# Kernel tuning notes

Measured on AMD Instinct MI355X. Metric: run time of the kernel, lower is better.

Reference implementation:

```python
import jax, jax.numpy as jnp
import numpy as np

EPS = 1e-6


def setup_inputs() -> dict:
    key = jax.random.key(0)
    k1, k2, k3 = jax.random.split(key, 3)
    B, L, H, D = 4, 4096, 16, 64
    return {
        "queries": jax.random.normal(k1, (B, L, H, D), dtype=jnp.float32),
        "keys": jax.random.normal(k2, (B, L, H, D), dtype=jnp.float32),
        "values": jax.random.normal(k3, (B, L, H, D), dtype=jnp.float32),
        "attn_mask": jnp.zeros((1,), dtype=bool),  # unused, matches torch signature
    }


def reference(queries, keys, values, attn_mask):
    # [B, L, H, D] -> [B, H, L, D]
    q = jax.nn.sigmoid(jnp.transpose(queries, (0, 2, 1, 3)))
    k = jax.nn.sigmoid(jnp.transpose(keys, (0, 2, 1, 3)))
    v = jnp.transpose(values, (0, 2, 1, 3))
    L = q.shape[2]
    S = k.shape[2]

    # flow normalizers (incoming / outgoing)
    normalizer_row = 1.0 / jnp.einsum('nhld,nhd->nhl', q + EPS, k.sum(axis=2) + EPS)
    normalizer_col = 1.0 / jnp.einsum('nhsd,nhd->nhs', k + EPS, q.sum(axis=2) + EPS)

    # competitive refinement
    row_refine = jnp.einsum(
        'nhld,nhd->nhl', q + EPS, (k * normalizer_col[..., None]).sum(axis=2) + EPS)
    col_refine = jnp.einsum(
        'nhsd,nhd->nhs', k + EPS, (q * normalizer_row[..., None]).sum(axis=2) + EPS)
    row_refine = jax.nn.sigmoid(row_refine * (float(L) / float(S)))
    col_refine = jax.nn.softmax(col_refine, axis=-1) * S

    # kv: [B, H, D, D]
    kv = jnp.einsum('nhsd,nhse->nhde', k, v * col_refine[..., None])
    x = jnp.einsum('nhld,nhde->nhle', q, kv)
    x = x * normalizer_row[..., None] * row_refine[..., None]
    # back to [B, L, H, D]
    return jnp.transpose(x, (0, 2, 1, 3))
```

## Files before the change

kernel.cpp:

```cpp
#include <hip/hip_runtime.h>
#include <math.h>
#include <stdint.h>

#define B_ 4
#define L_ 4096
#define H_ 16
#define EPSF 1e-6f
#define STR 66
#define STRO 68

typedef short bf16x8 __attribute__((ext_vector_type(8)));
typedef float f32x4 __attribute__((ext_vector_type(4)));
union FragU { uint32_t u[4]; bf16x8 v; };

__device__ __forceinline__ float sigf(float x) { return 1.0f / (1.0f + __expf(-x)); }

__device__ __forceinline__ uint32_t packhl(float x) {
    uint32_t xb = __float_as_uint(x);
    uint32_t hb = xb & 0xFFFF0000u;
    float lo = x - __uint_as_float(hb);
    return (hb >> 16) | (__float_as_uint(lo) & 0xFFFF0000u);
}

__device__ __forceinline__ void buildfrag(const uint32_t w[8], bf16x8& hi, bf16x8& lo) {
    FragU H, L;
#pragma unroll
    for (int t = 0; t < 4; ++t) {
        H.u[t] = __builtin_amdgcn_perm(w[2 * t + 1], w[2 * t], 0x05040100u);
        L.u[t] = __builtin_amdgcn_perm(w[2 * t + 1], w[2 * t], 0x07060302u);
    }
    hi = H.v; lo = L.v;
}

#define MFMA3(acc, ahi, alo, bhi, blo)                                        \
    acc = __builtin_amdgcn_mfma_f32_16x16x32_bf16(ahi, bhi, acc, 0, 0, 0);    \
    acc = __builtin_amdgcn_mfma_f32_16x16x32_bf16(ahi, blo, acc, 0, 0, 0);    \
    acc = __builtin_amdgcn_mfma_f32_16x16x32_bf16(alo, bhi, acc, 0, 0, 0);

__global__ __launch_bounds__(256) void k_ksum(const float* __restrict__ K,
                                              float* __restrict__ ksum) {
    int bh = blockIdx.x, b = bh >> 4, h = bh & 15;
    int t = threadIdx.x, lane = t & 63, w = t >> 6;
    int q4 = lane >> 4, i16 = lane & 15;
    int r0 = blockIdx.y * 256 + w * 64;
    float a0 = 0.f, a1 = 0.f, a2 = 0.f, a3 = 0.f;
    for (int it = 0; it < 16; ++it) {
        int r = r0 + it * 4 + q4;
        float4 x = *(const float4*)(K + (((size_t)b * L_ + r) * H_ + h) * 64 + 4 * i16);
        a0 += sigf(x.x); a1 += sigf(x.y); a2 += sigf(x.z); a3 += sigf(x.w);
    }
#pragma unroll
    for (int m = 16; m < 64; m <<= 1) {
        a0 += __shfl_xor(a0, m, 64); a1 += __shfl_xor(a1, m, 64);
        a2 += __shfl_xor(a2, m, 64); a3 += __shfl_xor(a3, m, 64);
    }
    if (q4 == 0) {
        atomicAdd(&ksum[bh * 64 + 4 * i16 + 0], a0);
        atomicAdd(&ksum[bh * 64 + 4 * i16 + 1], a1);
        atomicAdd(&ksum[bh * 64 + 4 * i16 + 2], a2);
        atomicAdd(&ksum[bh * 64 + 4 * i16 + 3], a3);
    }
}

__global__ __launch_bounds__(256) void k_qpass(const float* __restrict__ Q,
                                               const float* __restrict__ ksum,
                                               float* __restrict__ qsum,
                                               float* __restrict__ qn) {
    int bh = blockIdx.x, b = bh >> 4, h = bh & 15;
    int t = threadIdx.x, lane = t & 63, w = t >> 6;
    int q4 = lane >> 4, i16 = lane & 15;
    int r0 = blockIdx.y * 256 + w * 64;
    float4 ks4 = *(const float4*)(ksum + bh * 64 + 4 * i16);
    ks4.x += EPSF; ks4.y += EPSF; ks4.z += EPSF; ks4.w += EPSF;
    float qs0 = 0.f, qs1 = 0.f, qs2 = 0.f, qs3 = 0.f;
    float qa0 = 0.f, qa1 = 0.f, qa2 = 0.f, qa3 = 0.f;
    for (int it = 0; it < 16; ++it) {
        int r = r0 + it * 4 + q4;
        float4 x = *(const float4*)(Q + (((size_t)b * L_ + r) * H_ + h) * 64 + 4 * i16);
        float s0 = sigf(x.x), s1 = sigf(x.y), s2 = sigf(x.z), s3 = sigf(x.w);
        float pa = (s0 + EPSF) * ks4.x + (s1 + EPSF) * ks4.y +
                   (s2 + EPSF) * ks4.z + (s3 + EPSF) * ks4.w;
#pragma unroll
        for (int m = 1; m < 16; m <<= 1) pa += __shfl_xor(pa, m, 64);
        float nr = __builtin_amdgcn_rcpf(pa);
        qs0 += s0; qs1 += s1; qs2 += s2; qs3 += s3;
        qa0 += s0 * nr; qa1 += s1 * nr; qa2 += s2 * nr; qa3 += s3 * nr;
    }
#pragma unroll
    for (int m = 16; m < 64; m <<= 1) {
        qs0 += __shfl_xor(qs0, m, 64); qs1 += __shfl_xor(qs1, m, 64);
        qs2 += __shfl_xor(qs2, m, 64); qs3 += __shfl_xor(qs3, m, 64);
        qa0 += __shfl_xor(qa0, m, 64); qa1 += __shfl_xor(qa1, m, 64);
        qa2 += __shfl_xor(qa2, m, 64); qa3 += __shfl_xor(qa3, m, 64);
    }
    if (q4 == 0) {
        atomicAdd(&qsum[bh * 64 + 4 * i16 + 0], qs0);
        atomicAdd(&qsum[bh * 64 + 4 * i16 + 1], qs1);
        atomicAdd(&qsum[bh * 64 + 4 * i16 + 2], qs2);
        atomicAdd(&qsum[bh * 64 + 4 * i16 + 3], qs3);
        atomicAdd(&qn[bh * 64 + 4 * i16 + 0], qa0);
        atomicAdd(&qn[bh * 64 + 4 * i16 + 1], qa1);
        atomicAdd(&qn[bh * 64 + 4 * i16 + 2], qa2);
        atomicAdd(&qn[bh * 64 + 4 * i16 + 3], qa3);
    }
}

__global__ __launch_bounds__(256) void k_kv(const float* __restrict__ K,
                                            const float* __restrict__ V,
                                            const float* __restrict__ qsum,
                                            const float* __restrict__ qn,
                                            float* __restrict__ kn,
                                            float* __restrict__ den,
                                            float* __restrict__ KVg) {
    int bh = blockIdx.x, b = bh >> 4, h = bh & 15;
    int t = threadIdx.x, lane = t & 63, w = t >> 6;
    int q4 = lane >> 4, i16 = lane & 15;
    __shared__ uint32_t skp[64 * STR];
    __shared__ uint32_t vwp[64 * STR];
    float4 qsE = *(const float4*)(qsum + bh * 64 + 4 * i16);
    float4 qnE = *(const float4*)(qn + bh * 64 + 4 * i16);
    qsE.x += EPSF; qsE.y += EPSF; qsE.z += EPSF; qsE.w += EPSF;
    qnE.x += EPSF; qnE.y += EPSF; qnE.z += EPSF; qnE.w += EPSF;
    f32x4 acc[4];
#pragma unroll
    for (int tm = 0; tm < 4; ++tm) acc[tm] = (f32x4){0.f, 0.f, 0.f, 0.f};
    float kn0 = 0.f, kn1 = 0.f, kn2 = 0.f, kn3 = 0.f, dacc = 0.f;
    int rowbase = blockIdx.y * 256;
    for (int tile = 0; tile < 4; ++tile) {
#pragma unroll
        for (int j = 0; j < 4; ++j) {
            int lr = w * 16 + j * 4 + q4;
            int r = rowbase + tile * 64 + lr;
            size_t off = (((size_t)b * L_ + r) * H_ + h) * 64 + 4 * i16;
            float4 kx = *(const float4*)(K + off);
            float s0 = sigf(kx.x), s1 = sigf(kx.y), s2 = sigf(kx.z), s3 = sigf(kx.w);
            float pa = (s0 + EPSF) * qsE.x + (s1 + EPSF) * qsE.y +
                       (s2 + EPSF) * qsE.z + (s3 + EPSF) * qsE.w;
            float pc = (s0 + EPSF) * qnE.x + (s1 + EPSF) * qnE.y +
                       (s2 + EPSF) * qnE.z + (s3 + EPSF) * qnE.w;
#pragma unroll
            for (int m = 1; m < 16; m <<= 1) {
                pa += __shfl_xor(pa, m, 64);
                pc += __shfl_xor(pc, m, 64);
            }
            float ncol = __builtin_amdgcn_rcpf(pa);
            float es = __expf(pc);
            kn0 += s0 * ncol; kn1 += s1 * ncol; kn2 += s2 * ncol; kn3 += s3 * ncol;
            if (i16 == 0) dacc += es;
            uint32_t* sp = &skp[lr * STR + 4 * i16];
            *(uint2*)sp = make_uint2(packhl(s0), packhl(s1));
            *(uint2*)(sp + 2) = make_uint2(packhl(s2), packhl(s3));
            float4 vx = *(const float4*)(V + off);
            uint32_t* vp = &vwp[lr * STR + 4 * i16];
            *(uint2*)vp = make_uint2(packhl(vx.x * es), packhl(vx.y * es));
            *(uint2*)(vp + 2) = make_uint2(packhl(vx.z * es), packhl(vx.w * es));
        }
        __syncthreads();
#pragma unroll
        for (int ks = 0; ks < 2; ++ks) {
            uint32_t bw[8];
#pragma unroll
            for (int j = 0; j < 8; ++j)
                bw[j] = vwp[(32 * ks + 8 * q4 + j) * STR + 16 * w + i16];
            bf16x8 bhi, blo; buildfrag(bw, bhi, blo);
#pragma unroll
            for (int tm = 0; tm < 4; ++tm) {
                uint32_t aw[8];
#pragma unroll
                for (int j = 0; j < 8; ++j)
                    aw[j] = skp[(32 * ks + 8 * q4 + j) * STR + 16 * tm + i16];
                bf16x8 ahi, alo; buildfrag(aw, ahi, alo);
                MFMA3(acc[tm], ahi, alo, bhi, blo);
            }
        }
        __syncthreads();
    }
#pragma unroll
    for (int tm = 0; tm < 4; ++tm)
#pragma unroll
        for (int r = 0; r < 4; ++r)
            atomicAdd(&KVg[(size_t)bh * 4096 + (16 * tm + 4 * q4 + r) * 64 + 16 * w + i16],
                      acc[tm][r]);
#pragma unroll
    for (int m = 16; m < 64; m <<= 1) {
        kn0 += __shfl_xor(kn0, m, 64); kn1 += __shfl_xor(kn1, m, 64);
        kn2 += __shfl_xor(kn2, m, 64); kn3 += __shfl_xor(kn3, m, 64);
    }
    if (q4 == 0) {
        atomicAdd(&kn[bh * 64 + 4 * i16 + 0], kn0);
        atomicAdd(&kn[bh * 64 + 4 * i16 + 1], kn1);
        atomicAdd(&kn[bh * 64 + 4 * i16 + 2], kn2);
        atomicAdd(&kn[bh * 64 + 4 * i16 + 3], kn3);
    }
#pragma unroll
    for (int m = 1; m < 64; m <<= 1) dacc += __shfl_xor(dacc, m, 64);
    if (lane == 0) atomicAdd(&den[bh], dacc);
}

__global__ __launch_bounds__(256) void k_out(const float* __restrict__ Q,
                                             const float* __restrict__ ksum,
                                             const float* __restrict__ kn,
                                             const float* __restrict__ den,
                                             const float* __restrict__ KVg,
                                             float* __restrict__ out) {
    int bh = blockIdx.x, b = bh >> 4, h = bh & 15;
    int t = threadIdx.x, lane = t & 63, w = t >> 6;
    int q4 = lane >> 4, i16 = lane & 15;
    __shared__ uint32_t kvt[64 * STRO];
    __shared__ uint32_t sqp[4][16 * STRO];
    __shared__ float scale_s[4][16];
    float4 ksE = *(const float4*)(ksum + bh * 64 + 4 * i16);
    float4 knE = *(const float4*)(kn + bh * 64 + 4 * i16);
    ksE.x += EPSF; ksE.y += EPSF; ksE.z += EPSF; ksE.w += EPSF;
    knE.x += EPSF; knE.y += EPSF; knE.z += EPSF; knE.w += EPSF;
    float sden = 4096.0f * __builtin_amdgcn_rcpf(den[bh]);
    for (int idx = t; idx < 4096; idx += 256) {
        float x = KVg[(size_t)bh * 4096 + idx];
        kvt[(idx & 63) * STRO + (idx >> 6)] = packhl(x);
    }
    __syncthreads();
    int rowbase = blockIdx.y * 256;
    for (int g = 0; g < 4; ++g) {
        int r0 = rowbase + w * 64 + g * 16;
#pragma unroll
        for (int j = 0; j < 4; ++j) {
            int lr = j * 4 + q4;
            int r = r0 + lr;
            float4 qx = *(const float4*)(Q + (((size_t)b * L_ + r) * H_ + h) * 64 + 4 * i16);
            float s0 = sigf(qx.x), s1 = sigf(qx.y), s2 = sigf(qx.z), s3 = sigf(qx.w);
            float pa = (s0 + EPSF) * ksE.x + (s1 + EPSF) * ksE.y +
                       (s2 + EPSF) * ksE.z + (s3 + EPSF) * ksE.w;
            float pb = (s0 + EPSF) * knE.x + (s1 + EPSF) * knE.y +
                       (s2 + EPSF) * knE.z + (s3 + EPSF) * knE.w;
#pragma unroll
            for (int m = 1; m < 16; m <<= 1) {
                pa += __shfl_xor(pa, m, 64);
                pb += __shfl_xor(pb, m, 64);
            }
            float sc = __builtin_amdgcn_rcpf(pa) * sigf(pb) * sden;
            if (i16 == 0) scale_s[w][lr] = sc;
            uint32_t* sp = &sqp[w][lr * STRO + 4 * i16];
            *(uint4*)sp = make_uint4(packhl(s0), packhl(s1), packhl(s2), packhl(s3));
        }
        f32x4 acc[4];
#pragma unroll
        for (int tn = 0; tn < 4; ++tn) acc[tn] = (f32x4){0.f, 0.f, 0.f, 0.f};
#pragma unroll
        for (int ks = 0; ks < 2; ++ks) {
            const uint32_t* ap = &sqp[w][i16 * STRO + 32 * ks + 8 * q4];
            uint4 a0 = *(const uint4*)ap, a1 = *(const uint4*)(ap + 4);
            uint32_t aw[8] = {a0.x, a0.y, a0.z, a0.w, a1.x, a1.y, a1.z, a1.w};
            bf16x8 ahi, alo; buildfrag(aw, ahi, alo);
#pragma unroll
            for (int tn = 0; tn < 4; ++tn) {
                const uint32_t* bp = &kvt[(16 * tn + i16) * STRO + 32 * ks + 8 * q4];
                uint4 b0 = *(const uint4*)bp, b1 = *(const uint4*)(bp + 4);
                uint32_t bw[8] = {b0.x, b0.y, b0.z, b0.w, b1.x, b1.y, b1.z, b1.w};
                bf16x8 bhi, blo; buildfrag(bw, bhi, blo);
                MFMA3(acc[tn], ahi, alo, bhi, blo);
            }
        }
#pragma unroll
        for (int tn = 0; tn < 4; ++tn)
#pragma unroll
            for (int r = 0; r < 4; ++r) {
                int rl = 4 * q4 + r;
                float sc = scale_s[w][rl];
                out[(((size_t)b * L_ + (r0 + rl)) * H_ + h) * 64 + 16 * tn + i16] =
                    acc[tn][r] * sc;
            }
    }
}

extern "C" void kernel_launch(void* const* d_in, const int* in_sizes, int n_in,
                              void* d_out, int out_size, void* d_ws, size_t ws_size,
                              hipStream_t stream) {
    const float* Q = (const float*)d_in[0];
    const float* K = (const float*)d_in[1];
    const float* V = (const float*)d_in[2];
    float* out = (float*)d_out;
    float* ws = (float*)d_ws;
    float* ksum = ws;
    float* qsum = ws + 4096;
    float* qn   = ws + 8192;
    float* kn   = ws + 12288;
    float* den  = ws + 16384;
    float* KVg  = ws + 16448;

    hipMemsetAsync(d_ws, 0, (16448ull + 262144ull) * 4ull, stream);
    k_ksum<<<dim3(64, 16), 256, 0, stream>>>(K, ksum);
    k_qpass<<<dim3(64, 16), 256, 0, stream>>>(Q, ksum, qsum, qn);
    k_kv<<<dim3(64, 16), 256, 0, stream>>>(K, V, qsum, qn, kn, den, KVg);
    k_out<<<dim3(64, 16), 256, 0, stream>>>(Q, ksum, kn, den, KVg, out);
}
```

Baseline: 309.5 us.

## Prefetch tiles in registers, replace KV atomics with partial-sum reduce, double grid

Doubles the grid for the ksum/qpass kernels with batched float4 loads to raise memory-level parallelism. k_kv and k_out now prefetch the next tile's K/V or Q into registers while the current tile computes. The KV atomicAdd accumulation is replaced by per-block partial slices plus a separate reduce kernel, which also shrinks the memset. Adds launch-bounds occupancy hints, an extra kernel launch, 4 MB more workspace traffic, and more register pressure.

```diff
diff --git a/kernel.cpp b/kernel.cpp
--- a/kernel.cpp
+++ b/kernel.cpp
@@ -37,17 +37,26 @@
     acc = __builtin_amdgcn_mfma_f32_16x16x32_bf16(ahi, blo, acc, 0, 0, 0);    \
     acc = __builtin_amdgcn_mfma_f32_16x16x32_bf16(alo, bhi, acc, 0, 0, 0);
 
-__global__ __launch_bounds__(256) void k_ksum(const float* __restrict__ K,
-                                              float* __restrict__ ksum) {
+__global__ __launch_bounds__(256, 8) void k_ksum(const float* __restrict__ K,
+                                                 float* __restrict__ ksum) {
     int bh = blockIdx.x, b = bh >> 4, h = bh & 15;
     int t = threadIdx.x, lane = t & 63, w = t >> 6;
     int q4 = lane >> 4, i16 = lane & 15;
-    int r0 = blockIdx.y * 256 + w * 64;
+    int r0 = blockIdx.y * 128 + w * 32;
     float a0 = 0.f, a1 = 0.f, a2 = 0.f, a3 = 0.f;
-    for (int it = 0; it < 16; ++it) {
-        int r = r0 + it * 4 + q4;
-        float4 x = *(const float4*)(K + (((size_t)b * L_ + r) * H_ + h) * 64 + 4 * i16);
-        a0 += sigf(x.x); a1 += sigf(x.y); a2 += sigf(x.z); a3 += sigf(x.w);
+#pragma unroll
+    for (int ib = 0; ib < 2; ++ib) {
+        float4 x[4];
+#pragma unroll
+        for (int j = 0; j < 4; ++j) {
+            int r = r0 + (ib * 4 + j) * 4 + q4;
+            x[j] = *(const float4*)(K + (((size_t)b * L_ + r) * H_ + h) * 64 + 4 * i16);
+        }
+#pragma unroll
+        for (int j = 0; j < 4; ++j) {
+            a0 += sigf(x[j].x); a1 += sigf(x[j].y);
+            a2 += sigf(x[j].z); a3 += sigf(x[j].w);
+        }
     }
 #pragma unroll
     for (int m = 16; m < 64; m <<= 1) {
@@ -62,29 +71,37 @@
     }
 }
 
-__global__ __launch_bounds__(256) void k_qpass(const float* __restrict__ Q,
-                                               const float* __restrict__ ksum,
-                                               float* __restrict__ qsum,
-                                               float* __restrict__ qn) {
+__global__ __launch_bounds__(256, 6) void k_qpass(const float* __restrict__ Q,
+                                                  const float* __restrict__ ksum,
+                                                  float* __restrict__ qsum,
+                                                  float* __restrict__ qn) {
     int bh = blockIdx.x, b = bh >> 4, h = bh & 15;
     int t = threadIdx.x, lane = t & 63, w = t >> 6;
     int q4 = lane >> 4, i16 = lane & 15;
-    int r0 = blockIdx.y * 256 + w * 64;
+    int r0 = blockIdx.y * 128 + w * 32;
     float4 ks4 = *(const float4*)(ksum + bh * 64 + 4 * i16);
     ks4.x += EPSF; ks4.y += EPSF; ks4.z += EPSF; ks4.w += EPSF;
     float qs0 = 0.f, qs1 = 0.f, qs2 = 0.f, qs3 = 0.f;
     float qa0 = 0.f, qa1 = 0.f, qa2 = 0.f, qa3 = 0.f;
-    for (int it = 0; it < 16; ++it) {
-        int r = r0 + it * 4 + q4;
-        float4 x = *(const float4*)(Q + (((size_t)b * L_ + r) * H_ + h) * 64 + 4 * i16);
-        float s0 = sigf(x.x), s1 = sigf(x.y), s2 = sigf(x.z), s3 = sigf(x.w);
-        float pa = (s0 + EPSF) * ks4.x + (s1 + EPSF) * ks4.y +
-                   (s2 + EPSF) * ks4.z + (s3 + EPSF) * ks4.w;
-#pragma unroll
-        for (int m = 1; m < 16; m <<= 1) pa += __shfl_xor(pa, m, 64);
-        float nr = __builtin_amdgcn_rcpf(pa);
-        qs0 += s0; qs1 += s1; qs2 += s2; qs3 += s3;
-        qa0 += s0 * nr; qa1 += s1 * nr; qa2 += s2 * nr; qa3 += s3 * nr;
+#pragma unroll
+    for (int ib = 0; ib < 2; ++ib) {
+        float4 x[4];
+#pragma unroll
+        for (int j = 0; j < 4; ++j) {
+            int r = r0 + (ib * 4 + j) * 4 + q4;
+            x[j] = *(const float4*)(Q + (((size_t)b * L_ + r) * H_ + h) * 64 + 4 * i16);
+        }
+#pragma unroll
+        for (int j = 0; j < 4; ++j) {
+            float s0 = sigf(x[j].x), s1 = sigf(x[j].y), s2 = sigf(x[j].z), s3 = sigf(x[j].w);
+            float pa = (s0 + EPSF) * ks4.x + (s1 + EPSF) * ks4.y +
+                       (s2 + EPSF) * ks4.z + (s3 + EPSF) * ks4.w;
+#pragma unroll
+            for (int m = 1; m < 16; m <<= 1) pa += __shfl_xor(pa, m, 64);
+            float nr = __builtin_amdgcn_rcpf(pa);
+            qs0 += s0; qs1 += s1; qs2 += s2; qs3 += s3;
+            qa0 += s0 * nr; qa1 += s1 * nr; qa2 += s2 * nr; qa3 += s3 * nr;
+        }
     }
 #pragma unroll
     for (int m = 16; m < 64; m <<= 1) {
@@ -105,13 +122,13 @@
     }
 }
 
-__global__ __launch_bounds__(256) void k_kv(const float* __restrict__ K,
-                                            const float* __restrict__ V,
-                                            const float* __restrict__ qsum,
-                                            const float* __restrict__ qn,
-                                            float* __restrict__ kn,
-                                            float* __restrict__ den,
-                                            float* __restrict__ KVg) {
+__global__ __launch_bounds__(256, 4) void k_kv(const float* __restrict__ K,
+                                               const float* __restrict__ V,
+                                               const float* __restrict__ qsum,
+                                               const float* __restrict__ qn,
+                                               float* __restrict__ kn,
+                                               float* __restrict__ den,
+                                               float* __restrict__ KVp) {
     int bh = blockIdx.x, b = bh >> 4, h = bh & 15;
     int t = threadIdx.x, lane = t & 63, w = t >> 6;
     int q4 = lane >> 4, i16 = lane & 15;
@@ -126,14 +143,20 @@
     for (int tm = 0; tm < 4; ++tm) acc[tm] = (f32x4){0.f, 0.f, 0.f, 0.f};
     float kn0 = 0.f, kn1 = 0.f, kn2 = 0.f, kn3 = 0.f, dacc = 0.f;
     int rowbase = blockIdx.y * 256;
+    float4 kx[4], vx[4];
+#pragma unroll
+    for (int j = 0; j < 4; ++j) {
+        int r = rowbase + w * 16 + j * 4 + q4;
+        size_t off = (((size_t)b * L_ + r) * H_ + h) * 64 + 4 * i16;
+        kx[j] = *(const float4*)(K + off);
+        vx[j] = *(const float4*)(V + off);
+    }
+#pragma unroll
     for (int tile = 0; tile < 4; ++tile) {
 #pragma unroll
         for (int j = 0; j < 4; ++j) {
             int lr = w * 16 + j * 4 + q4;
-            int r = rowbase + tile * 64 + lr;
-            size_t off = (((size_t)b * L_ + r) * H_ + h) * 64 + 4 * i16;
-            float4 kx = *(const float4*)(K + off);
-            float s0 = sigf(kx.x), s1 = sigf(kx.y), s2 = sigf(kx.z), s3 = sigf(kx.w);
+            float s0 = sigf(kx[j].x), s1 = sigf(kx[j].y), s2 = sigf(kx[j].z), s3 = sigf(kx[j].w);
             float pa = (s0 + EPSF) * qsE.x + (s1 + EPSF) * qsE.y +
                        (s2 + EPSF) * qsE.z + (s3 + EPSF) * qsE.w;
             float pc = (s0 + EPSF) * qnE.x + (s1 + EPSF) * qnE.y +
@@ -150,10 +173,19 @@
             uint32_t* sp = &skp[lr * STR + 4 * i16];
             *(uint2*)sp = make_uint2(packhl(s0), packhl(s1));
             *(uint2*)(sp + 2) = make_uint2(packhl(s2), packhl(s3));
-            float4 vx = *(const float4*)(V + off);
             uint32_t* vp = &vwp[lr * STR + 4 * i16];
-            *(uint2*)vp = make_uint2(packhl(vx.x * es), packhl(vx.y * es));
-            *(uint2*)(vp + 2) = make_uint2(packhl(vx.z * es), packhl(vx.w * es));
+            *(uint2*)vp = make_uint2(packhl(vx[j].x * es), packhl(vx[j].y * es));
+            *(uint2*)(vp + 2) = make_uint2(packhl(vx[j].z * es), packhl(vx[j].w * es));
+        }
+        float4 kx2[4], vx2[4];
+        if (tile < 3) {
+#pragma unroll
+            for (int j = 0; j < 4; ++j) {
+                int r = rowbase + (tile + 1) * 64 + w * 16 + j * 4 + q4;
+                size_t off = (((size_t)b * L_ + r) * H_ + h) * 64 + 4 * i16;
+                kx2[j] = *(const float4*)(K + off);
+                vx2[j] = *(const float4*)(V + off);
+            }
         }
         __syncthreads();
 #pragma unroll
@@ -174,13 +206,17 @@
             }
         }
         __syncthreads();
-    }
+        if (tile < 3) {
+#pragma unroll
+            for (int j = 0; j < 4; ++j) { kx[j] = kx2[j]; vx[j] = vx2[j]; }
+        }
+    }
+    float* kvslice = KVp + ((size_t)blockIdx.y * 64 + bh) * 4096;
 #pragma unroll
     for (int tm = 0; tm < 4; ++tm)
 #pragma unroll
         for (int r = 0; r < 4; ++r)
-            atomicAdd(&KVg[(size_t)bh * 4096 + (16 * tm + 4 * q4 + r) * 64 + 16 * w + i16],
-                      acc[tm][r]);
+            kvslice[(16 * tm + 4 * q4 + r) * 64 + 16 * w + i16] = acc[tm][r];
 #pragma unroll
     for (int m = 16; m < 64; m <<= 1) {
         kn0 += __shfl_xor(kn0, m, 64); kn1 += __shfl_xor(kn1, m, 64);
@@ -197,12 +233,25 @@
     if (lane == 0) atomicAdd(&den[bh], dacc);
 }
 
-__global__ __launch_bounds__(256) void k_out(const float* __restrict__ Q,
-                                             const float* __restrict__ ksum,
-                                             const float* __restrict__ kn,
-                                             const float* __restrict__ den,
-                                             const float* __restrict__ KVg,
-                                             float* __restrict__ out) {
+__global__ __launch_bounds__(256) void k_reduce(const float* __restrict__ KVp,
+                                                float* __restrict__ KVg) {
+    int bh = blockIdx.x;
+    int f4 = blockIdx.y * 256 + threadIdx.x;
+    float4 acc = make_float4(0.f, 0.f, 0.f, 0.f);
+#pragma unroll
+    for (int p = 0; p < 16; ++p) {
+        float4 x = *(const float4*)(KVp + ((size_t)p * 64 + bh) * 4096 + 4 * f4);
+        acc.x += x.x; acc.y += x.y; acc.z += x.z; acc.w += x.w;
+    }
+    *(float4*)(KVg + (size_t)bh * 4096 + 4 * f4) = acc;
+}
+
+__global__ __launch_bounds__(256, 4) void k_out(const float* __restrict__ Q,
+                                                const float* __restrict__ ksum,
+                                                const float* __restrict__ kn,
+                                                const float* __restrict__ den,
+                                                const float* __restrict__ KVg,
+                                                float* __restrict__ out) {
     int bh = blockIdx.x, b = bh >> 4, h = bh & 15;
     int t = threadIdx.x, lane = t & 63, w = t >> 6;
     int q4 = lane >> 4, i16 = lane & 15;
@@ -214,20 +263,31 @@
     ksE.x += EPSF; ksE.y += EPSF; ksE.z += EPSF; ksE.w += EPSF;
     knE.x += EPSF; knE.y += EPSF; knE.z += EPSF; knE.w += EPSF;
     float sden = 4096.0f * __builtin_amdgcn_rcpf(den[bh]);
-    for (int idx = t; idx < 4096; idx += 256) {
-        float x = KVg[(size_t)bh * 4096 + idx];
-        kvt[(idx & 63) * STRO + (idx >> 6)] = packhl(x);
+#pragma unroll
+    for (int i = 0; i < 4; ++i) {
+        int f4 = t + i * 256;
+        float4 x = *(const float4*)(KVg + (size_t)bh * 4096 + 4 * f4);
+        int d = (4 * f4) & 63, e = f4 >> 4;
+        kvt[(d + 0) * STRO + e] = packhl(x.x);
+        kvt[(d + 1) * STRO + e] = packhl(x.y);
+        kvt[(d + 2) * STRO + e] = packhl(x.z);
+        kvt[(d + 3) * STRO + e] = packhl(x.w);
+    }
+    int rowbase = blockIdx.y * 256;
+    float4 qx[4];
+#pragma unroll
+    for (int j = 0; j < 4; ++j) {
+        int r = rowbase + w * 64 + j * 4 + q4;
+        qx[j] = *(const float4*)(Q + (((size_t)b * L_ + r) * H_ + h) * 64 + 4 * i16);
     }
     __syncthreads();
-    int rowbase = blockIdx.y * 256;
+#pragma unroll
     for (int g = 0; g < 4; ++g) {
         int r0 = rowbase + w * 64 + g * 16;
 #pragma unroll
         for (int j = 0; j < 4; ++j) {
             int lr = j * 4 + q4;
-            int r = r0 + lr;
-            float4 qx = *(const float4*)(Q + (((size_t)b * L_ + r) * H_ + h) * 64 + 4 * i16);
-            float s0 = sigf(qx.x), s1 = sigf(qx.y), s2 = sigf(qx.z), s3 = sigf(qx.w);
+            float s0 = sigf(qx[j].x), s1 = sigf(qx[j].y), s2 = sigf(qx[j].z), s3 = sigf(qx[j].w);
             float pa = (s0 + EPSF) * ksE.x + (s1 + EPSF) * ksE.y +
                        (s2 + EPSF) * ksE.z + (s3 + EPSF) * ksE.w;
             float pb = (s0 + EPSF) * knE.x + (s1 + EPSF) * knE.y +
@@ -241,6 +301,14 @@
             if (i16 == 0) scale_s[w][lr] = sc;
             uint32_t* sp = &sqp[w][lr * STRO + 4 * i16];
             *(uint4*)sp = make_uint4(packhl(s0), packhl(s1), packhl(s2), packhl(s3));
+        }
+        float4 qx2[4];
+        if (g < 3) {
+#pragma unroll
+            for (int j = 0; j < 4; ++j) {
+                int r = rowbase + w * 64 + (g + 1) * 16 + j * 4 + q4;
+                qx2[j] = *(const float4*)(Q + (((size_t)b * L_ + r) * H_ + h) * 64 + 4 * i16);
+            }
         }
         f32x4 acc[4];
 #pragma unroll
@@ -269,6 +337,10 @@
                 out[(((size_t)b * L_ + (r0 + rl)) * H_ + h) * 64 + 16 * tn + i16] =
                     acc[tn][r] * sc;
             }
+        if (g < 3) {
+#pragma unroll
+            for (int j = 0; j < 4; ++j) qx[j] = qx2[j];
+        }
     }
 }
 
@@ -286,10 +358,12 @@
     float* kn   = ws + 12288;
     float* den  = ws + 16384;
     float* KVg  = ws + 16448;
-
-    hipMemsetAsync(d_ws, 0, (16448ull + 262144ull) * 4ull, stream);
-    k_ksum<<<dim3(64, 16), 256, 0, stream>>>(K, ksum);
-    k_qpass<<<dim3(64, 16), 256, 0, stream>>>(Q, ksum, qsum, qn);
-    k_kv<<<dim3(64, 16), 256, 0, stream>>>(K, V, qsum, qn, kn, den, KVg);
+    float* KVp  = ws + 16448 + 262144;
+
+    hipMemsetAsync(d_ws, 0, 16448ull * 4ull, stream);
+    k_ksum<<<dim3(64, 32), 256, 0, stream>>>(K, ksum);
+    k_qpass<<<dim3(64, 32), 256, 0, stream>>>(Q, ksum, qsum, qn);
+    k_kv<<<dim3(64, 16), 256, 0, stream>>>(K, V, qsum, qn, kn, den, KVp);
+    k_reduce<<<dim3(64, 4), 256, 0, stream>>>(KVp, KVg);
     k_out<<<dim3(64, 16), 256, 0, stream>>>(Q, ksum, kn, den, KVg, out);
 }
```

Result: no change. 308.2 us (-0.4%).
